# Optimization experiments

Measured on AMD Instinct MI355X. Metric: run time of the kernel, lower is better.

## Reference

```python
import jax, jax.numpy as jnp
import numpy as np

POOL_SIZE = 7


def setup_inputs() -> dict:
    key = jax.random.key(0)
    k1, k2, k3 = jax.random.split(key, 3)
    B, H, W, C = 1, 128, 128, 1024
    N = 512
    shared_layers = jax.random.normal(k1, (B, H, W, C), dtype=jnp.float32)
    # Build valid boxes [ymin, xmin, ymax, xmax] with min <= max, inside the map.
    mins = jax.random.uniform(k2, (N, 2), minval=0.0, maxval=float(H - 2))
    spans = jax.random.uniform(k3, (N, 2), minval=1.0, maxval=32.0)
    maxs = jnp.minimum(mins + spans, float(H - 1))
    rois = jnp.stack([mins[:, 0], mins[:, 1], maxs[:, 0], maxs[:, 1]], axis=1).astype(jnp.float32)
    return {"shared_layers": shared_layers, "rois": rois}


def reference(shared_layers, rois):
    """Per-ROI crop + bilinear resize (TF1 resize_bilinear, align_corners=False),
    concatenated over ROIs then flattened. Fully vectorized over ROIs."""
    P = POOL_SIZE
    B, H, W, C = shared_layers.shape  # B == 1 as in the original usage
    feat = shared_layers[0]  # [H, W, C]

    ymin = rois[:, 0].astype(jnp.int32)
    xmin = rois[:, 1].astype(jnp.int32)
    ymax = rois[:, 2].astype(jnp.int32)
    xmax = rois[:, 3].astype(jnp.int32)
    h = (ymax - ymin + 1).astype(jnp.float32)  # [N]
    w = (xmax - xmin + 1).astype(jnp.float32)

    grid = jnp.arange(P, dtype=jnp.float32)  # [P]
    # TF resize_bilinear (align_corners=False): src = out_idx * in_size / out_size
    src_y = grid[None, :] * (h[:, None] / P)  # [N, P]
    src_x = grid[None, :] * (w[:, None] / P)  # [N, P]

    y0 = jnp.floor(src_y).astype(jnp.int32)
    x0 = jnp.floor(src_x).astype(jnp.int32)
    y1 = jnp.minimum(y0 + 1, (ymax - ymin)[:, None])
    x1 = jnp.minimum(x0 + 1, (xmax - xmin)[:, None])
    fy = (src_y - y0.astype(jnp.float32))[:, :, None, None]  # [N, P, 1, 1]
    fx = (src_x - x0.astype(jnp.float32))[:, None, :, None]  # [N, 1, P, 1]

    gy0 = ymin[:, None] + y0  # [N, P] global row indices
    gy1 = ymin[:, None] + y1
    gx0 = xmin[:, None] + x0  # [N, P] global col indices
    gx1 = xmin[:, None] + x1

    # 4 corner gathers -> [N, P, P, C]
    tl = feat[gy0[:, :, None], gx0[:, None, :]]
    tr = feat[gy0[:, :, None], gx1[:, None, :]]
    bl = feat[gy1[:, :, None], gx0[:, None, :]]
    br = feat[gy1[:, :, None], gx1[:, None, :]]

    top = tl + (tr - tl) * fx
    bot = bl + (br - bl) * fx
    out = top + (bot - top) * fy  # [N, P, P, C]

    return out.reshape(out.shape[0], -1)  # Flatten -> [N, P*P*C]
```

## Files before the change

kernel.cpp:

```cpp
#include <hip/hip_runtime.h>


#define POOL_P 7
#define FEAT_C 1024
#define FEAT_W 128

__global__ __launch_bounds__(256) void roi_pool_kernel(
    const float* __restrict__ feat,
    const float* __restrict__ rois,
    float* __restrict__ out)
{
    const int blk = blockIdx.x;
    const int px  = blk % POOL_P;
    const int py  = (blk / POOL_P) % POOL_P;
    const int r   = blk / (POOL_P * POOL_P);

    const float4 roi = ((const float4*)rois)[r];
    const int ymin = (int)roi.x;
    const int xmin = (int)roi.y;
    const int ymax = (int)roi.z;
    const int xmax = (int)roi.w;

    const float h = (float)(ymax - ymin + 1);
    const float w = (float)(xmax - xmin + 1);

    const float src_y = (float)py * (h / 7.0f);
    const float src_x = (float)px * (w / 7.0f);

    const int y0 = (int)floorf(src_y);
    const int x0 = (int)floorf(src_x);
    const int y1 = min(y0 + 1, ymax - ymin);
    const int x1 = min(x0 + 1, xmax - xmin);

    const float fy = src_y - (float)y0;
    const float fx = src_x - (float)x0;

    const int gy0 = ymin + y0;
    const int gy1 = ymin + y1;
    const int gx0 = xmin + x0;
    const int gx1 = xmin + x1;

    const float4* __restrict__ tlp = (const float4*)(feat + ((size_t)(gy0 * FEAT_W + gx0)) * FEAT_C);
    const float4* __restrict__ trp = (const float4*)(feat + ((size_t)(gy0 * FEAT_W + gx1)) * FEAT_C);
    const float4* __restrict__ blp = (const float4*)(feat + ((size_t)(gy1 * FEAT_W + gx0)) * FEAT_C);
    const float4* __restrict__ brp = (const float4*)(feat + ((size_t)(gy1 * FEAT_W + gx1)) * FEAT_C);
    float4* __restrict__ op = (float4*)(out + (size_t)blk * FEAT_C);

    const int t = threadIdx.x;

    const float4 tl = tlp[t];
    const float4 tr = trp[t];
    const float4 bl = blp[t];
    const float4 br = brp[t];

    float4 res;
    {
        float top, bot;
        top = tl.x + (tr.x - tl.x) * fx;
        bot = bl.x + (br.x - bl.x) * fx;
        res.x = top + (bot - top) * fy;
        top = tl.y + (tr.y - tl.y) * fx;
        bot = bl.y + (br.y - bl.y) * fx;
        res.y = top + (bot - top) * fy;
        top = tl.z + (tr.z - tl.z) * fx;
        bot = bl.z + (br.z - bl.z) * fx;
        res.z = top + (bot - top) * fy;
        top = tl.w + (tr.w - tl.w) * fx;
        bot = bl.w + (br.w - bl.w) * fx;
        res.w = top + (bot - top) * fy;
    }
    op[t] = res;
}

extern "C" void kernel_launch(void* const* d_in, const int* in_sizes, int n_in,
                              void* d_out, int out_size, void* d_ws, size_t ws_size,
                              hipStream_t stream) {
    const float* feat = (const float*)d_in[0];
    const float* rois = (const float*)d_in[1];
    float* out        = (float*)d_out;

    const int n_rois  = in_sizes[1] / 4;
    const int n_blocks = n_rois * POOL_P * POOL_P;

    roi_pool_kernel<<<n_blocks, 256, 0, stream>>>(feat, rois, out);
}
```

Measured before the change: 181.1 us.

## Interleave ROIs across block order and halve block size with two float4s per thread

Block indices are remapped so that consecutive blocks cover the same pooling cell of 8 different ROIs, not all 49 cells of one ROI. This spreads concurrent gathers across more distinct feature rows and output regions, which may change cache and channel locality. Blocks shrink from 256 to 128 threads, and each thread now loads and writes two float4 chunks to raise memory-level parallelism. The remap assumes the ROI count is a multiple of 8; otherwise blocks would index past the end of the ROI array.

```diff
diff --git a/kernel.cpp b/kernel.cpp
--- a/kernel.cpp
+++ b/kernel.cpp
@@ -4,16 +4,21 @@
 #define POOL_P 7
 #define FEAT_C 1024
 #define FEAT_W 128
+#define CELLS_PER_ROI (POOL_P * POOL_P)
+#define GROUP_BLOCKS  (8 * CELLS_PER_ROI)
 
-__global__ __launch_bounds__(256) void roi_pool_kernel(
+__global__ __launch_bounds__(128) void roi_pool_kernel(
     const float* __restrict__ feat,
     const float* __restrict__ rois,
     float* __restrict__ out)
 {
-    const int blk = blockIdx.x;
-    const int px  = blk % POOL_P;
-    const int py  = (blk / POOL_P) % POOL_P;
-    const int r   = blk / (POOL_P * POOL_P);
+    const int i    = blockIdx.x;
+    const int q    = i / GROUP_BLOCKS;
+    const int k    = i - q * GROUP_BLOCKS;
+    const int r    = 8 * q + (k & 7);
+    const int cell = k >> 3;
+    const int px   = cell % POOL_P;
+    const int py   = cell / POOL_P;
 
     const float4 roi = ((const float4*)rois)[r];
     const int ymin = (int)roi.x;
@@ -44,32 +49,34 @@
     const float4* __restrict__ trp = (const float4*)(feat + ((size_t)(gy0 * FEAT_W + gx1)) * FEAT_C);
     const float4* __restrict__ blp = (const float4*)(feat + ((size_t)(gy1 * FEAT_W + gx0)) * FEAT_C);
     const float4* __restrict__ brp = (const float4*)(feat + ((size_t)(gy1 * FEAT_W + gx1)) * FEAT_C);
-    float4* __restrict__ op = (float4*)(out + (size_t)blk * FEAT_C);
+    float4* __restrict__ op = (float4*)(out + ((size_t)r * CELLS_PER_ROI + cell) * FEAT_C);
 
-    const int t = threadIdx.x;
+    const int t0 = threadIdx.x;
+    const int t1 = t0 + 128;
 
-    const float4 tl = tlp[t];
-    const float4 tr = trp[t];
-    const float4 bl = blp[t];
-    const float4 br = brp[t];
+    const float4 tl0 = tlp[t0];
+    const float4 tr0 = trp[t0];
+    const float4 bl0 = blp[t0];
+    const float4 br0 = brp[t0];
+    const float4 tl1 = tlp[t1];
+    const float4 tr1 = trp[t1];
+    const float4 bl1 = blp[t1];
+    const float4 br1 = brp[t1];
 
-    float4 res;
+    float4 res0, res1;
     {
         float top, bot;
-        top = tl.x + (tr.x - tl.x) * fx;
-        bot = bl.x + (br.x - bl.x) * fx;
-        res.x = top + (bot - top) * fy;
-        top = tl.y + (tr.y - tl.y) * fx;
-        bot = bl.y + (br.y - bl.y) * fx;
-        res.y = top + (bot - top) * fy;
-        top = tl.z + (tr.z - tl.z) * fx;
-        bot = bl.z + (br.z - bl.z) * fx;
-        res.z = top + (bot - top) * fy;
-        top = tl.w + (tr.w - tl.w) * fx;
-        bot = bl.w + (br.w - bl.w) * fx;
-        res.w = top + (bot - top) * fy;
+        top = tl0.x + (tr0.x - tl0.x) * fx; bot = bl0.x + (br0.x - bl0.x) * fx; res0.x = top + (bot - top) * fy;
+        top = tl0.y + (tr0.y - tl0.y) * fx; bot = bl0.y + (br0.y - bl0.y) * fx; res0.y = top + (bot - top) * fy;
+        top = tl0.z + (tr0.z - tl0.z) * fx; bot = bl0.z + (br0.z - bl0.z) * fx; res0.z = top + (bot - top) * fy;
+        top = tl0.w + (tr0.w - tl0.w) * fx; bot = bl0.w + (br0.w - bl0.w) * fx; res0.w = top + (bot - top) * fy;
+        top = tl1.x + (tr1.x - tl1.x) * fx; bot = bl1.x + (br1.x - bl1.x) * fx; res1.x = top + (bot - top) * fy;
+        top = tl1.y + (tr1.y - tl1.y) * fx; bot = bl1.y + (br1.y - bl1.y) * fx; res1.y = top + (bot - top) * fy;
+        top = tl1.z + (tr1.z - tl1.z) * fx; bot = bl1.z + (br1.z - bl1.z) * fx; res1.z = top + (bot - top) * fy;
+        top = tl1.w + (tr1.w - tl1.w) * fx; bot = bl1.w + (br1.w - bl1.w) * fx; res1.w = top + (bot - top) * fy;
     }
-    op[t] = res;
+    op[t0] = res0;
+    op[t1] = res1;
 }
 
 extern "C" void kernel_launch(void* const* d_in, const int* in_sizes, int n_in,
@@ -79,8 +86,8 @@
     const float* rois = (const float*)d_in[1];
     float* out        = (float*)d_out;
 
-    const int n_rois  = in_sizes[1] / 4;
-    const int n_blocks = n_rois * POOL_P * POOL_P;
+    const int n_rois   = in_sizes[1] / 4;
+    const int n_blocks = n_rois * CELLS_PER_ROI;
 
-    roi_pool_kernel<<<n_blocks, 256, 0, stream>>>(feat, rois, out);
+    roi_pool_kernel<<<n_blocks, 128, 0, stream>>>(feat, rois, out);
 }
```

New measurement: 170.8 us. 1.06x faster.

## Sort ROIs by ymin and map sorted chunks to XCDs for L2 locality

Applied to the files above, without the earlier changes.

Adds a small ranking kernel that sorts ROIs by ymin into a permutation held in workspace. The pooling kernel then remaps block indices so each XCD (assumed 8, with round-robin block dispatch) handles a contiguous range of sorted ROIs, so spatially nearby ROIs share feature rows in that XCD's L2. It also halves the block size with each thread processing two float4s, and uses nontemporal stores for the output. The extra kernel launch and the O(n^2) single-block rank add overhead and assume n_rois <= 512.

```diff
diff --git a/kernel.cpp b/kernel.cpp
--- a/kernel.cpp
+++ b/kernel.cpp
@@ -4,16 +4,47 @@
 #define POOL_P 7
 #define FEAT_C 1024
 #define FEAT_W 128
+#define CELLS_PER_ROI (POOL_P * POOL_P)
+#define NUM_XCD 8
 
-__global__ __launch_bounds__(256) void roi_pool_kernel(
+typedef float nfloat4 __attribute__((ext_vector_type(4)));
+
+__global__ __launch_bounds__(512) void rank_rois_kernel(
+    const float* __restrict__ rois, int n, int* __restrict__ perm)
+{
+    __shared__ float ys[512];
+    const int t = threadIdx.x;
+    if (t < n) ys[t] = rois[4 * t];
+    __syncthreads();
+    if (t < n) {
+        const float y = ys[t];
+        int rank = 0;
+        for (int j = 0; j < n; ++j) {
+            const float yj = ys[j];
+            rank += (yj < y) || (yj == y && j < t);
+        }
+        perm[rank] = t;
+    }
+}
+
+__global__ __launch_bounds__(128) void roi_pool_kernel(
     const float* __restrict__ feat,
     const float* __restrict__ rois,
-    float* __restrict__ out)
+    const int* __restrict__ perm,
+    float* __restrict__ out,
+    int n_rois, int ranks_per_xcd)
 {
-    const int blk = blockIdx.x;
-    const int px  = blk % POOL_P;
-    const int py  = (blk / POOL_P) % POOL_P;
-    const int r   = blk / (POOL_P * POOL_P);
+    const int i = blockIdx.x;
+    const int k = i & (NUM_XCD - 1);
+    const int j = i >> 3;
+    const int rank_local = j / CELLS_PER_ROI;
+    const int cell = j - rank_local * CELLS_PER_ROI;
+    const int rank = k * ranks_per_xcd + rank_local;
+    if (rank >= n_rois) return;
+    const int r = perm[rank];
+
+    const int px = cell % POOL_P;
+    const int py = cell / POOL_P;
 
     const float4 roi = ((const float4*)rois)[r];
     const int ymin = (int)roi.x;
@@ -40,36 +71,33 @@
     const int gx0 = xmin + x0;
     const int gx1 = xmin + x1;
 
-    const float4* __restrict__ tlp = (const float4*)(feat + ((size_t)(gy0 * FEAT_W + gx0)) * FEAT_C);
-    const float4* __restrict__ trp = (const float4*)(feat + ((size_t)(gy0 * FEAT_W + gx1)) * FEAT_C);
-    const float4* __restrict__ blp = (const float4*)(feat + ((size_t)(gy1 * FEAT_W + gx0)) * FEAT_C);
-    const float4* __restrict__ brp = (const float4*)(feat + ((size_t)(gy1 * FEAT_W + gx1)) * FEAT_C);
-    float4* __restrict__ op = (float4*)(out + (size_t)blk * FEAT_C);
+    const nfloat4* __restrict__ tlp = (const nfloat4*)(feat + ((size_t)(gy0 * FEAT_W + gx0)) * FEAT_C);
+    const nfloat4* __restrict__ trp = (const nfloat4*)(feat + ((size_t)(gy0 * FEAT_W + gx1)) * FEAT_C);
+    const nfloat4* __restrict__ blp = (const nfloat4*)(feat + ((size_t)(gy1 * FEAT_W + gx0)) * FEAT_C);
+    const nfloat4* __restrict__ brp = (const nfloat4*)(feat + ((size_t)(gy1 * FEAT_W + gx1)) * FEAT_C);
+    nfloat4* __restrict__ op = (nfloat4*)(out + ((size_t)r * CELLS_PER_ROI + cell) * FEAT_C);
 
-    const int t = threadIdx.x;
+    const int t0 = threadIdx.x;
+    const int t1 = t0 + 128;
 
-    const float4 tl = tlp[t];
-    const float4 tr = trp[t];
-    const float4 bl = blp[t];
-    const float4 br = brp[t];
+    const nfloat4 tl0 = tlp[t0];
+    const nfloat4 tr0 = trp[t0];
+    const nfloat4 bl0 = blp[t0];
+    const nfloat4 br0 = brp[t0];
+    const nfloat4 tl1 = tlp[t1];
+    const nfloat4 tr1 = trp[t1];
+    const nfloat4 bl1 = blp[t1];
+    const nfloat4 br1 = brp[t1];
 
-    float4 res;
-    {
-        float top, bot;
-        top = tl.x + (tr.x - tl.x) * fx;
-        bot = bl.x + (br.x - bl.x) * fx;
-        res.x = top + (bot - top) * fy;
-        top = tl.y + (tr.y - tl.y) * fx;
-        bot = bl.y + (br.y - bl.y) * fx;
-        res.y = top + (bot - top) * fy;
-        top = tl.z + (tr.z - tl.z) * fx;
-        bot = bl.z + (br.z - bl.z) * fx;
-        res.z = top + (bot - top) * fy;
-        top = tl.w + (tr.w - tl.w) * fx;
-        bot = bl.w + (br.w - bl.w) * fx;
-        res.w = top + (bot - top) * fy;
-    }
-    op[t] = res;
+    nfloat4 top0 = tl0 + (tr0 - tl0) * fx;
+    nfloat4 bot0 = bl0 + (br0 - bl0) * fx;
+    nfloat4 res0 = top0 + (bot0 - top0) * fy;
+    nfloat4 top1 = tl1 + (tr1 - tl1) * fx;
+    nfloat4 bot1 = bl1 + (br1 - bl1) * fx;
+    nfloat4 res1 = top1 + (bot1 - top1) * fy;
+
+    __builtin_nontemporal_store(res0, &op[t0]);
+    __builtin_nontemporal_store(res1, &op[t1]);
 }
 
 extern "C" void kernel_launch(void* const* d_in, const int* in_sizes, int n_in,
@@ -78,9 +106,13 @@
     const float* feat = (const float*)d_in[0];
     const float* rois = (const float*)d_in[1];
     float* out        = (float*)d_out;
+    int*   perm       = (int*)d_ws;
 
-    const int n_rois  = in_sizes[1] / 4;
-    const int n_blocks = n_rois * POOL_P * POOL_P;
+    const int n_rois        = in_sizes[1] / 4;
+    const int ranks_per_xcd = (n_rois + NUM_XCD - 1) / NUM_XCD;
+    const int n_blocks      = NUM_XCD * ranks_per_xcd * CELLS_PER_ROI;
 
-    roi_pool_kernel<<<n_blocks, 256, 0, stream>>>(feat, rois, out);
+    rank_rois_kernel<<<1, 512, 0, stream>>>(rois, n_rois, perm);
+    roi_pool_kernel<<<n_blocks, 128, 0, stream>>>(feat, rois, perm, out,
+                                                  n_rois, ranks_per_xcd);
 }
```

Result: no change. 179.6 us (-0.8%).

## Process a full pooled row per block with software-prefetched corner loads

Applied to the files above, without the earlier changes.

Each block now computes all 7 output cells of one pooled row for a ROI instead of a single cell, and loads the next cell's four corners before doing the current cell's math. Block indices are interleaved across groups of 8 ROIs, and outputs are written with nontemporal stores. The aim is to cut per-block launch overhead, keep more loads in flight, and avoid polluting cache with output data. In exchange there are 7x fewer blocks and higher register use, and the grid assumes the ROI count is a multiple of 8.

```diff
diff --git a/kernel.cpp b/kernel.cpp
--- a/kernel.cpp
+++ b/kernel.cpp
@@ -4,16 +4,21 @@
 #define POOL_P 7
 #define FEAT_C 1024
 #define FEAT_W 128
+#define CELLS_PER_ROI (POOL_P * POOL_P)
+#define ROWS_PER_GROUP (8 * POOL_P)
 
-__global__ __launch_bounds__(256) void roi_pool_kernel(
+typedef float nfloat4 __attribute__((ext_vector_type(4)));
+
+__global__ __launch_bounds__(256) void roi_pool_row_kernel(
     const float* __restrict__ feat,
     const float* __restrict__ rois,
     float* __restrict__ out)
 {
-    const int blk = blockIdx.x;
-    const int px  = blk % POOL_P;
-    const int py  = (blk / POOL_P) % POOL_P;
-    const int r   = blk / (POOL_P * POOL_P);
+    const int i  = blockIdx.x;
+    const int q  = i / ROWS_PER_GROUP;
+    const int k  = i - q * ROWS_PER_GROUP;
+    const int r  = 8 * q + (k & 7);
+    const int py = k >> 3;
 
     const float4 roi = ((const float4*)rois)[r];
     const int ymin = (int)roi.x;
@@ -25,51 +30,56 @@
     const float w = (float)(xmax - xmin + 1);
 
     const float src_y = (float)py * (h / 7.0f);
-    const float src_x = (float)px * (w / 7.0f);
+    const int   y0    = (int)floorf(src_y);
+    const int   y1    = min(y0 + 1, ymax - ymin);
+    const float fy    = src_y - (float)y0;
 
-    const int y0 = (int)floorf(src_y);
-    const int x0 = (int)floorf(src_x);
-    const int y1 = min(y0 + 1, ymax - ymin);
-    const int x1 = min(x0 + 1, xmax - xmin);
+    const float* __restrict__ row0 = feat + (size_t)((ymin + y0) * FEAT_W) * FEAT_C;
+    const float* __restrict__ row1 = feat + (size_t)((ymin + y1) * FEAT_W) * FEAT_C;
 
-    const float fy = src_y - (float)y0;
-    const float fx = src_x - (float)x0;
-
-    const int gy0 = ymin + y0;
-    const int gy1 = ymin + y1;
-    const int gx0 = xmin + x0;
-    const int gx1 = xmin + x1;
-
-    const float4* __restrict__ tlp = (const float4*)(feat + ((size_t)(gy0 * FEAT_W + gx0)) * FEAT_C);
-    const float4* __restrict__ trp = (const float4*)(feat + ((size_t)(gy0 * FEAT_W + gx1)) * FEAT_C);
-    const float4* __restrict__ blp = (const float4*)(feat + ((size_t)(gy1 * FEAT_W + gx0)) * FEAT_C);
-    const float4* __restrict__ brp = (const float4*)(feat + ((size_t)(gy1 * FEAT_W + gx1)) * FEAT_C);
-    float4* __restrict__ op = (float4*)(out + (size_t)blk * FEAT_C);
+    const float wdiv7 = w / 7.0f;
+    const int   xspan = xmax - xmin;
 
     const int t = threadIdx.x;
+    float* __restrict__ outp = out + ((size_t)r * CELLS_PER_ROI + (size_t)py * POOL_P) * FEAT_C;
 
-    const float4 tl = tlp[t];
-    const float4 tr = trp[t];
-    const float4 bl = blp[t];
-    const float4 br = brp[t];
+    auto calcx = [&](int px, int& gx0, int& gx1, float& fx) {
+        const float sx = (float)px * wdiv7;
+        const int   x0 = (int)floorf(sx);
+        const int   x1 = min(x0 + 1, xspan);
+        fx  = sx - (float)x0;
+        gx0 = xmin + x0;
+        gx1 = xmin + x1;
+    };
 
-    float4 res;
-    {
-        float top, bot;
-        top = tl.x + (tr.x - tl.x) * fx;
-        bot = bl.x + (br.x - bl.x) * fx;
-        res.x = top + (bot - top) * fy;
-        top = tl.y + (tr.y - tl.y) * fx;
-        bot = bl.y + (br.y - bl.y) * fx;
-        res.y = top + (bot - top) * fy;
-        top = tl.z + (tr.z - tl.z) * fx;
-        bot = bl.z + (br.z - bl.z) * fx;
-        res.z = top + (bot - top) * fy;
-        top = tl.w + (tr.w - tl.w) * fx;
-        bot = bl.w + (br.w - bl.w) * fx;
-        res.w = top + (bot - top) * fy;
+    int gx0, gx1; float fx;
+    calcx(0, gx0, gx1, fx);
+    nfloat4 tl = ((const nfloat4*)(row0 + (size_t)gx0 * FEAT_C))[t];
+    nfloat4 tr = ((const nfloat4*)(row0 + (size_t)gx1 * FEAT_C))[t];
+    nfloat4 bl = ((const nfloat4*)(row1 + (size_t)gx0 * FEAT_C))[t];
+    nfloat4 br = ((const nfloat4*)(row1 + (size_t)gx1 * FEAT_C))[t];
+
+#pragma unroll
+    for (int px = 0; px < POOL_P; ++px) {
+        nfloat4 ntl, ntr, nbl, nbr; float nfx = 0.f;
+        if (px < POOL_P - 1) {
+            int ngx0, ngx1;
+            calcx(px + 1, ngx0, ngx1, nfx);
+            ntl = ((const nfloat4*)(row0 + (size_t)ngx0 * FEAT_C))[t];
+            ntr = ((const nfloat4*)(row0 + (size_t)ngx1 * FEAT_C))[t];
+            nbl = ((const nfloat4*)(row1 + (size_t)ngx0 * FEAT_C))[t];
+            nbr = ((const nfloat4*)(row1 + (size_t)ngx1 * FEAT_C))[t];
+        }
+
+        const nfloat4 top = tl + (tr - tl) * fx;
+        const nfloat4 bot = bl + (br - bl) * fx;
+        const nfloat4 res = top + (bot - top) * fy;
+        __builtin_nontemporal_store(res, &((nfloat4*)(outp + (size_t)px * FEAT_C))[t]);
+
+        if (px < POOL_P - 1) {
+            tl = ntl; tr = ntr; bl = nbl; br = nbr; fx = nfx;
+        }
     }
-    op[t] = res;
 }
 
 extern "C" void kernel_launch(void* const* d_in, const int* in_sizes, int n_in,
@@ -79,8 +89,8 @@
     const float* rois = (const float*)d_in[1];
     float* out        = (float*)d_out;
 
-    const int n_rois  = in_sizes[1] / 4;
-    const int n_blocks = n_rois * POOL_P * POOL_P;
+    const int n_rois   = in_sizes[1] / 4;
+    const int n_blocks = n_rois * POOL_P;
 
-    roi_pool_kernel<<<n_blocks, 256, 0, stream>>>(feat, rois, out);
+    roi_pool_row_kernel<<<n_blocks, 256, 0, stream>>>(feat, rois, out);
 }
```

New measurement: 173.1 us. 4.4% less time.
